# Kernel tuning notes

Hardware: AMD Instinct MI355X
Metric: run time of the kernel (lower is better)

The kernel has to match this reference:

```python
import jax, jax.numpy as jnp
import numpy as np

CAR_DIM = 8
ESC_MAX_AGENT = 32
HID = 256
ACTION_DIM = 30
NUM_STATES = 64
BATCH = 8192
ENC_OUT = 1 + CAR_DIM * ESC_MAX_AGENT          # 257
Q_IN = 1 + CAR_DIM + CAR_DIM * ESC_MAX_AGENT   # 265


def setup_inputs() -> dict:
    key = jax.random.key(0)
    ks = jax.random.split(key, 9)
    s = jax.random.normal(ks[0], (BATCH, CAR_DIM + NUM_STATES * CAR_DIM), dtype=jnp.float32)
    def lin(k, fan_in, fan_out):
        bound = 1.0 / np.sqrt(fan_in)
        kw, kb = jax.random.split(k)
        W = jax.random.uniform(kw, (fan_in, fan_out), jnp.float32, -bound, bound)
        b = jax.random.uniform(kb, (fan_out,), jnp.float32, -bound, bound)
        return W, b
    W1, b1 = lin(ks[1], CAR_DIM, HID)
    W2, b2 = lin(ks[2], HID, ENC_OUT)
    Qw1, Qb1 = lin(ks[3], Q_IN, HID)
    Qw2, Qb2 = lin(ks[4], HID, ACTION_DIM)
    return {"s": s, "W1": W1, "b1": b1, "W2": W2, "b2": b2,
            "Qw1": Qw1, "Qb1": Qb1, "Qw2": Qw2, "Qb2": Qb2}


def reference(s, W1, b1, W2, b2, Qw1, Qb1, Qw2, Qb2):
    B = s.shape[0]
    self_states = s[:, :CAR_DIM]                                   # [B, C]
    surr = s[:, CAR_DIM:].reshape(B, -1, CAR_DIM)                  # [B, N, C]
    # sentinel agents: any coordinate exactly == -1 is skipped
    valid = ~jnp.any(surr == -1.0, axis=-1)                        # [B, N] bool
    h = jax.nn.relu(jnp.einsum('bnc,ch->bnh', surr, W1) + b1)      # [B, N, HID]
    enc = jax.nn.relu(jnp.einsum('bnh,he->bne', h, W2) + b2)       # [B, N, ENC_OUT]
    sum_outputs = jnp.sum(enc * valid[:, :, None].astype(enc.dtype), axis=1)  # [B, ENC_OUT]
    x = jnp.concatenate([self_states, sum_outputs], axis=1)        # [B, Q_IN]
    q = jax.nn.relu(x @ Qw1 + Qb1) @ Qw2 + Qb2                     # [B, ACTION_DIM]
    return q
```

## Files before the change

kernel.cpp:

```cpp
#include <hip/hip_runtime.h>

#define CAR 8
#define SROW 520
#define HID 256
#define EOUT 257
#define XPAD 288
#define ADIM 30

typedef __attribute__((ext_vector_type(8))) short sh8;
typedef __attribute__((ext_vector_type(4))) float f32x4;

__device__ __forceinline__ short f2bf(float f) {
  unsigned u = __builtin_bit_cast(unsigned, f);
  u += 0x7fffu + ((u >> 16) & 1u);
  return (short)(u >> 16);
}
__device__ __forceinline__ unsigned f2bf2(float a, float b) {
  unsigned ua = __builtin_bit_cast(unsigned, a);
  ua += 0x7fffu + ((ua >> 16) & 1u);
  unsigned ub = __builtin_bit_cast(unsigned, b);
  ub += 0x7fffu + ((ub >> 16) & 1u);
  return __builtin_amdgcn_perm(ub, ua, 0x07060302);
}

__global__ void k_prep(const float* __restrict__ W1, const float* __restrict__ W2,
                       const float* __restrict__ Qw1, const float* __restrict__ Qw2,
                       short* __restrict__ w1f, short* __restrict__ w2f,
                       short* __restrict__ w3f, short* __restrict__ wq2f) {
  int idx = blockIdx.x * 256 + threadIdx.x;
  if (idx < 8192) {
    int mt = idx >> 9, r = idx & 511, lane = r >> 3, j = r & 7;
    int quad = lane >> 4, m = lane & 15;
    float v = (quad == 0) ? W1[j * HID + mt * 16 + m] : 0.0f;
    w1f[idx] = f2bf(v);
    return;
  }
  int i2 = idx - 8192;
  if (i2 < 69632) {
    int ks = i2 / 8704, r = i2 % 8704;
    int nt = r >> 9, r2 = r & 511, lane = r2 >> 3, j = r2 & 7;
    int quad = lane >> 4, m = lane & 15;
    int k = ks * 32 + quad * 8 + j, n = nt * 16 + m;
    float v = (n < EOUT) ? W2[k * EOUT + n] : 0.0f;
    w2f[i2] = f2bf(v);
    return;
  }
  int i3 = i2 - 69632;
  if (i3 < 73728) {
    int ks = i3 >> 13, r = i3 & 8191;
    int nt = r >> 9, r2 = r & 511, lane = r2 >> 3, j = r2 & 7;
    int quad = lane >> 4, m = lane & 15;
    int k = ks * 32 + quad * 8 + j, n = nt * 16 + m;
    float v = (k < 265) ? Qw1[k * HID + n] : 0.0f;
    w3f[i3] = f2bf(v);
    return;
  }
  int i4 = i3 - 73728;
  if (i4 < 8192) {
    int ks = i4 >> 10, r = i4 & 1023;
    int nt = r >> 9, r2 = r & 511, lane = r2 >> 3, j = r2 & 7;
    int quad = lane >> 4, m = lane & 15;
    int k = ks * 32 + quad * 8 + j, n = nt * 16 + m;
    float v = (n < ADIM) ? Qw2[k * ADIM + n] : 0.0f;
    wq2f[i4] = f2bf(v);
  }
}

__global__ __launch_bounds__(256, 2)
void k_enc(const float* __restrict__ s, const short* __restrict__ w1f,
           const float* __restrict__ b1, const short* __restrict__ w2f,
           const float* __restrict__ b2, float* __restrict__ so288) {
  __shared__ short hlds[16384];
  __shared__ float ninvp[4];

  const int b = blockIdx.x;
  const int tid = threadIdx.x;
  const int w = tid >> 6, lane = tid & 63;
  const int q = lane >> 4, m = lane & 15;
  const float* srow0 = s + (size_t)b * SROW + CAR;

  sh8 bs = {0, 0, 0, 0, 0, 0, 0, 0};
  bool inv = false;
  if (q == 0) {
    const float* sr = srow0 + (w * 16 + m) * CAR;
    float4 f0 = ((const float4*)sr)[0], f1 = ((const float4*)sr)[1];
    inv = (f0.x == -1.f) | (f0.y == -1.f) | (f0.z == -1.f) | (f0.w == -1.f) |
          (f1.x == -1.f) | (f1.y == -1.f) | (f1.z == -1.f) | (f1.w == -1.f);
    unsigned u0 = f2bf2(f0.x, f0.y), u1 = f2bf2(f0.z, f0.w);
    unsigned u2 = f2bf2(f1.x, f1.y), u3 = f2bf2(f1.z, f1.w);
    int4 t = {(int)u0, (int)u1, (int)u2, (int)u3};
    bs = __builtin_bit_cast(sh8, t);
  }
  const float vflag = inv ? 0.f : 1.f;
  const float vv = __shfl(vflag, m, 64);
  unsigned long long bal = __ballot(inv);
  if (lane == 0) ninvp[w] = (float)__popcll(bal);

#pragma unroll
  for (int mt = 0; mt < 16; ++mt) {
    sh8 af = *(const sh8*)(w1f + (mt * 64 + lane) * 8);
    f32x4 z = {0.f, 0.f, 0.f, 0.f};
    f32x4 c = __builtin_amdgcn_mfma_f32_16x16x32_bf16(af, bs, z, 0, 0, 0);
    const int hidb = mt * 16 + q * 4;
    float4 b1v = *(const float4*)(b1 + hidb);
    const int ks = hidb >> 5, qB = (hidb >> 3) & 3, js = hidb & 7;
    unsigned p0 = f2bf2(fmaxf(c[0] + b1v.x, 0.f) * vv, fmaxf(c[1] + b1v.y, 0.f) * vv);
    unsigned p1 = f2bf2(fmaxf(c[2] + b1v.z, 0.f) * vv, fmaxf(c[3] + b1v.w, 0.f) * vv);
    uint2 pk = {p0, p1};
    *(uint2*)(hlds + ((w * 8 + ks) * 64 + qB * 16 + m) * 8 + js) = pk;
  }
  __syncthreads();

  const int NT = (w == 0) ? 5 : 4;
  int tiles[5];
#pragma unroll
  for (int i = 0; i < 4; ++i) tiles[i] = 4 * w + i;
  tiles[4] = 16;

  f32x4 acc[4][5];
#pragma unroll
  for (int mt = 0; mt < 4; ++mt)
#pragma unroll
    for (int i = 0; i < 5; ++i) {
      f32x4 z = {0.f, 0.f, 0.f, 0.f};
      acc[mt][i] = z;
    }

#pragma unroll
  for (int ks = 0; ks < 8; ++ks) {
    sh8 A[4];
#pragma unroll
    for (int mt = 0; mt < 4; ++mt)
      A[mt] = *(const sh8*)(hlds + ((mt * 8 + ks) * 64 + lane) * 8);
    sh8 Bf[5];
#pragma unroll
    for (int i = 0; i < 5; ++i)
      if (i < NT)
        Bf[i] = *(const sh8*)(w2f + ((ks * 17 + tiles[i]) * 64 + lane) * 8);
#pragma unroll
    for (int i = 0; i < 5; ++i)
      if (i < NT)
#pragma unroll
        for (int mt = 0; mt < 4; ++mt)
          acc[mt][i] = __builtin_amdgcn_mfma_f32_16x16x32_bf16(A[mt], Bf[i], acc[mt][i], 0, 0, 0);
  }

  const float ninv = ninvp[0] + ninvp[1] + ninvp[2] + ninvp[3];
#pragma unroll
  for (int i = 0; i < 5; ++i)
    if (i < NT) {
      const int col = tiles[i] * 16 + m;
      const float b2c = (col < EOUT) ? b2[col] : 0.f;
      float ssum = 0.f;
#pragma unroll
      for (int mt = 0; mt < 4; ++mt)
#pragma unroll
        for (int r = 0; r < 4; ++r)
          ssum += fmaxf(acc[mt][i][r] + b2c, 0.f);
      ssum += __shfl_xor(ssum, 16, 64);
      ssum += __shfl_xor(ssum, 32, 64);
      ssum -= ninv * fmaxf(b2c, 0.f);
      if (q == 0)
        so288[(size_t)b * XPAD + CAR + col] = ssum;
    }
  if (w == 1 && lane < CAR)
    so288[(size_t)b * XPAD + lane] = s[(size_t)b * SROW + lane];
  if (w == 2 && lane < 8)
    so288[(size_t)b * XPAD + 280 + lane] = 0.f;
}

__global__ __launch_bounds__(64, 2)
void k_q(const float* __restrict__ so288, const short* __restrict__ w3f,
         const float* __restrict__ Qb1, const short* __restrict__ wq2f,
         const float* __restrict__ Qb2, float* __restrict__ out, int B) {
  __shared__ float H[16 * 260];
  const int lane = threadIdx.x;
  const int q = lane >> 4, m = lane & 15;
  const int b0 = blockIdx.x * 16;
  int row = b0 + m; if (row >= B) row = B - 1;
  const float* xr = so288 + (size_t)row * XPAD;

  f32x4 acc1[16];
#pragma unroll
  for (int nt = 0; nt < 16; ++nt) {
    f32x4 z = {0.f, 0.f, 0.f, 0.f};
    acc1[nt] = z;
  }

#pragma unroll
  for (int ks = 0; ks < 9; ++ks) {
    const float* xp = xr + ks * 32 + q * 8;
    float4 xa = ((const float4*)xp)[0], xb = ((const float4*)xp)[1];
    unsigned u0 = f2bf2(xa.x, xa.y), u1 = f2bf2(xa.z, xa.w);
    unsigned u2 = f2bf2(xb.x, xb.y), u3 = f2bf2(xb.z, xb.w);
    int4 t = {(int)u0, (int)u1, (int)u2, (int)u3};
    sh8 A = __builtin_bit_cast(sh8, t);
#pragma unroll
    for (int nt = 0; nt < 16; ++nt) {
      sh8 Bf = *(const sh8*)(w3f + ((ks * 16 + nt) * 64 + lane) * 8);
      acc1[nt] = __builtin_amdgcn_mfma_f32_16x16x32_bf16(A, Bf, acc1[nt], 0, 0, 0);
    }
  }
#pragma unroll
  for (int nt = 0; nt < 16; ++nt) {
    const float bq = Qb1[nt * 16 + m];
#pragma unroll
    for (int r = 0; r < 4; ++r)
      H[(q * 4 + r) * 260 + nt * 16 + m] = fmaxf(acc1[nt][r] + bq, 0.f);
  }
  __syncthreads();

  f32x4 acc2[2];
#pragma unroll
  for (int nt = 0; nt < 2; ++nt) {
    f32x4 z = {0.f, 0.f, 0.f, 0.f};
    acc2[nt] = z;
  }
#pragma unroll
  for (int ks = 0; ks < 8; ++ks) {
    const float* hp = H + m * 260 + ks * 32 + q * 8;
    float4 ha = ((const float4*)hp)[0], hb = ((const float4*)hp)[1];
    unsigned u0 = f2bf2(ha.x, ha.y), u1 = f2bf2(ha.z, ha.w);
    unsigned u2 = f2bf2(hb.x, hb.y), u3 = f2bf2(hb.z, hb.w);
    int4 t = {(int)u0, (int)u1, (int)u2, (int)u3};
    sh8 A2 = __builtin_bit_cast(sh8, t);
#pragma unroll
    for (int nt = 0; nt < 2; ++nt) {
      sh8 Bf = *(const sh8*)(wq2f + ((ks * 2 + nt) * 64 + lane) * 8);
      acc2[nt] = __builtin_amdgcn_mfma_f32_16x16x32_bf16(A2, Bf, acc2[nt], 0, 0, 0);
    }
  }
#pragma unroll
  for (int nt = 0; nt < 2; ++nt) {
    const int act = nt * 16 + m;
    if (act < ADIM) {
      const float bq = Qb2[act];
#pragma unroll
      for (int r = 0; r < 4; ++r) {
        const int br = b0 + q * 4 + r;
        if (br < B) out[(size_t)br * ADIM + act] = acc2[nt][r] + bq;
      }
    }
  }
}

extern "C" void kernel_launch(void* const* d_in, const int* in_sizes, int n_in,
                              void* d_out, int out_size, void* d_ws, size_t ws_size,
                              hipStream_t stream) {
  const float* s   = (const float*)d_in[0];
  const float* W1  = (const float*)d_in[1];
  const float* b1  = (const float*)d_in[2];
  const float* W2  = (const float*)d_in[3];
  const float* b2  = (const float*)d_in[4];
  const float* Qw1 = (const float*)d_in[5];
  const float* Qb1 = (const float*)d_in[6];
  const float* Qw2 = (const float*)d_in[7];
  const float* Qb2 = (const float*)d_in[8];
  float* out = (float*)d_out;
  const int B = in_sizes[0] / SROW;

  char* wsb = (char*)d_ws;
  float* so288 = (float*)wsb;
  size_t off = (size_t)B * XPAD * sizeof(float);
  short* w1f  = (short*)(wsb + off);            off += 8192 * 2;
  short* w2f  = (short*)(wsb + off);            off += 69632 * 2;
  short* w3f  = (short*)(wsb + off);            off += 73728 * 2;
  short* wq2f = (short*)(wsb + off);

  const int prep_elems = 8192 + 69632 + 73728 + 8192;
  k_prep<<<(prep_elems + 255) / 256, 256, 0, stream>>>(W1, W2, Qw1, Qw2,
                                                       w1f, w2f, w3f, wq2f);
  k_enc<<<B, 256, 0, stream>>>(s, w1f, b1, w2f, b2, so288);
  k_q<<<(B + 15) / 16, 64, 0, stream>>>(so288, w3f, Qb1, wq2f, Qb2, out, B);
}
```

Baseline: 178.4 us.

## Process two batch rows per encoder block and widen Q-head blocks to 32 rows

k_enc now handles two batch elements per block, so each W2 fragment it loads is reused across both elements' hidden tiles. W2 fragments are also prefetched one k-step ahead. k_q moves from 64-thread/16-row blocks to 256-thread/32-row blocks, with the bf16-converted input staged in LDS and the Qw1 column tiles split across waves. This is meant to cut redundant weight traffic and raise per-block MFMA work, at the cost of more registers (acc doubles to 40 f32x4), more LDS, and a padded fifth W2 tile on non-zero waves that now costs extra MFMAs. k_enc also assumes an even B, since odd B is not guarded.

```diff
diff --git a/kernel.cpp b/kernel.cpp
--- a/kernel.cpp
+++ b/kernel.cpp
@@ -70,176 +70,216 @@
 void k_enc(const float* __restrict__ s, const short* __restrict__ w1f,
            const float* __restrict__ b1, const short* __restrict__ w2f,
            const float* __restrict__ b2, float* __restrict__ so288) {
-  __shared__ short hlds[16384];
+  __shared__ __align__(16) short hlds[2][16384];
   __shared__ float ninvp[4];
 
-  const int b = blockIdx.x;
   const int tid = threadIdx.x;
   const int w = tid >> 6, lane = tid & 63;
   const int q = lane >> 4, m = lane & 15;
-  const float* srow0 = s + (size_t)b * SROW + CAR;
-
-  sh8 bs = {0, 0, 0, 0, 0, 0, 0, 0};
+  const int be = w >> 1, half = w & 1;
+  const size_t b0 = 2 * (size_t)blockIdx.x;
+  const int bg = (int)b0 + be;
+
+  const float* srow0 = s + (size_t)bg * SROW + CAR;
+  int4 pk = {0, 0, 0, 0};
   bool inv = false;
-  if (q == 0) {
-    const float* sr = srow0 + (w * 16 + m) * CAR;
+  if (lane < 32) {
+    const float* sr = srow0 + (half * 32 + lane) * CAR;
     float4 f0 = ((const float4*)sr)[0], f1 = ((const float4*)sr)[1];
     inv = (f0.x == -1.f) | (f0.y == -1.f) | (f0.z == -1.f) | (f0.w == -1.f) |
           (f1.x == -1.f) | (f1.y == -1.f) | (f1.z == -1.f) | (f1.w == -1.f);
-    unsigned u0 = f2bf2(f0.x, f0.y), u1 = f2bf2(f0.z, f0.w);
-    unsigned u2 = f2bf2(f1.x, f1.y), u3 = f2bf2(f1.z, f1.w);
-    int4 t = {(int)u0, (int)u1, (int)u2, (int)u3};
-    bs = __builtin_bit_cast(sh8, t);
+    pk.x = (int)f2bf2(f0.x, f0.y); pk.y = (int)f2bf2(f0.z, f0.w);
+    pk.z = (int)f2bf2(f1.x, f1.y); pk.w = (int)f2bf2(f1.z, f1.w);
   }
   const float vflag = inv ? 0.f : 1.f;
-  const float vv = __shfl(vflag, m, 64);
   unsigned long long bal = __ballot(inv);
   if (lane == 0) ninvp[w] = (float)__popcll(bal);
 
+  int4 p0, p1;
+  p0.x = __shfl(pk.x, m, 64);      p0.y = __shfl(pk.y, m, 64);
+  p0.z = __shfl(pk.z, m, 64);      p0.w = __shfl(pk.w, m, 64);
+  p1.x = __shfl(pk.x, 16 + m, 64); p1.y = __shfl(pk.y, 16 + m, 64);
+  p1.z = __shfl(pk.z, 16 + m, 64); p1.w = __shfl(pk.w, 16 + m, 64);
+  const float vv0 = __shfl(vflag, m, 64);
+  const float vv1 = __shfl(vflag, 16 + m, 64);
+  if (q != 0) { p0.x = p0.y = p0.z = p0.w = 0; p1.x = p1.y = p1.z = p1.w = 0; }
+  sh8 bs0 = __builtin_bit_cast(sh8, p0);
+  sh8 bs1 = __builtin_bit_cast(sh8, p1);
+
+  const int T0 = half * 2, T1 = half * 2 + 1;
 #pragma unroll
   for (int mt = 0; mt < 16; ++mt) {
     sh8 af = *(const sh8*)(w1f + (mt * 64 + lane) * 8);
     f32x4 z = {0.f, 0.f, 0.f, 0.f};
-    f32x4 c = __builtin_amdgcn_mfma_f32_16x16x32_bf16(af, bs, z, 0, 0, 0);
+    f32x4 c0 = __builtin_amdgcn_mfma_f32_16x16x32_bf16(af, bs0, z, 0, 0, 0);
+    f32x4 c1 = __builtin_amdgcn_mfma_f32_16x16x32_bf16(af, bs1, z, 0, 0, 0);
     const int hidb = mt * 16 + q * 4;
     float4 b1v = *(const float4*)(b1 + hidb);
     const int ks = hidb >> 5, qB = (hidb >> 3) & 3, js = hidb & 7;
-    unsigned p0 = f2bf2(fmaxf(c[0] + b1v.x, 0.f) * vv, fmaxf(c[1] + b1v.y, 0.f) * vv);
-    unsigned p1 = f2bf2(fmaxf(c[2] + b1v.z, 0.f) * vv, fmaxf(c[3] + b1v.w, 0.f) * vv);
-    uint2 pk = {p0, p1};
-    *(uint2*)(hlds + ((w * 8 + ks) * 64 + qB * 16 + m) * 8 + js) = pk;
+    uint2 k0, k1;
+    k0.x = f2bf2(fmaxf(c0[0] + b1v.x, 0.f) * vv0, fmaxf(c0[1] + b1v.y, 0.f) * vv0);
+    k0.y = f2bf2(fmaxf(c0[2] + b1v.z, 0.f) * vv0, fmaxf(c0[3] + b1v.w, 0.f) * vv0);
+    k1.x = f2bf2(fmaxf(c1[0] + b1v.x, 0.f) * vv1, fmaxf(c1[1] + b1v.y, 0.f) * vv1);
+    k1.y = f2bf2(fmaxf(c1[2] + b1v.z, 0.f) * vv1, fmaxf(c1[3] + b1v.w, 0.f) * vv1);
+    *(uint2*)(&hlds[be][((T0 * 8 + ks) * 64 + qB * 16 + m) * 8 + js]) = k0;
+    *(uint2*)(&hlds[be][((T1 * 8 + ks) * 64 + qB * 16 + m) * 8 + js]) = k1;
   }
   __syncthreads();
 
-  const int NT = (w == 0) ? 5 : 4;
   int tiles[5];
 #pragma unroll
   for (int i = 0; i < 4; ++i) tiles[i] = 4 * w + i;
-  tiles[4] = 16;
-
-  f32x4 acc[4][5];
+  tiles[4] = (w == 0) ? 16 : 4 * w;
+
+  f32x4 acc[4][5][2];
 #pragma unroll
   for (int mt = 0; mt < 4; ++mt)
 #pragma unroll
-    for (int i = 0; i < 5; ++i) {
-      f32x4 z = {0.f, 0.f, 0.f, 0.f};
-      acc[mt][i] = z;
-    }
+    for (int i = 0; i < 5; ++i)
+#pragma unroll
+      for (int e = 0; e < 2; ++e) {
+        f32x4 z = {0.f, 0.f, 0.f, 0.f};
+        acc[mt][i][e] = z;
+      }
+
+  sh8 Bf[5];
+#pragma unroll
+  for (int i = 0; i < 5; ++i)
+    Bf[i] = *(const sh8*)(w2f + ((0 * 17 + tiles[i]) * 64 + lane) * 8);
 
 #pragma unroll
   for (int ks = 0; ks < 8; ++ks) {
-    sh8 A[4];
-#pragma unroll
-    for (int mt = 0; mt < 4; ++mt)
-      A[mt] = *(const sh8*)(hlds + ((mt * 8 + ks) * 64 + lane) * 8);
-    sh8 Bf[5];
-#pragma unroll
-    for (int i = 0; i < 5; ++i)
-      if (i < NT)
-        Bf[i] = *(const sh8*)(w2f + ((ks * 17 + tiles[i]) * 64 + lane) * 8);
-#pragma unroll
-    for (int i = 0; i < 5; ++i)
-      if (i < NT)
+    sh8 Bn[5];
+    if (ks < 7) {
+#pragma unroll
+      for (int i = 0; i < 5; ++i)
+        Bn[i] = *(const sh8*)(w2f + (((ks + 1) * 17 + tiles[i]) * 64 + lane) * 8);
+    }
+#pragma unroll
+    for (int e = 0; e < 2; ++e) {
+      sh8 A[4];
+#pragma unroll
+      for (int mt = 0; mt < 4; ++mt)
+        A[mt] = *(const sh8*)(&hlds[e][((mt * 8 + ks) * 64 + lane) * 8]);
+#pragma unroll
+      for (int i = 0; i < 5; ++i)
 #pragma unroll
         for (int mt = 0; mt < 4; ++mt)
-          acc[mt][i] = __builtin_amdgcn_mfma_f32_16x16x32_bf16(A[mt], Bf[i], acc[mt][i], 0, 0, 0);
-  }
-
-  const float ninv = ninvp[0] + ninvp[1] + ninvp[2] + ninvp[3];
-#pragma unroll
-  for (int i = 0; i < 5; ++i)
-    if (i < NT) {
-      const int col = tiles[i] * 16 + m;
-      const float b2c = (col < EOUT) ? b2[col] : 0.f;
+          acc[mt][i][e] = __builtin_amdgcn_mfma_f32_16x16x32_bf16(A[mt], Bf[i], acc[mt][i][e], 0, 0, 0);
+    }
+    if (ks < 7) {
+#pragma unroll
+      for (int i = 0; i < 5; ++i) Bf[i] = Bn[i];
+    }
+  }
+
+  const float ninv[2] = {ninvp[0] + ninvp[1], ninvp[2] + ninvp[3]};
+#pragma unroll
+  for (int i = 0; i < 5; ++i) {
+    if (i == 4 && w != 0) continue;
+    const int col = tiles[i] * 16 + m;
+    const float b2c = (col < EOUT) ? b2[col] : 0.f;
+    const float rb2 = fmaxf(b2c, 0.f);
+#pragma unroll
+    for (int e = 0; e < 2; ++e) {
       float ssum = 0.f;
 #pragma unroll
       for (int mt = 0; mt < 4; ++mt)
 #pragma unroll
         for (int r = 0; r < 4; ++r)
-          ssum += fmaxf(acc[mt][i][r] + b2c, 0.f);
+          ssum += fmaxf(acc[mt][i][e][r] + b2c, 0.f);
       ssum += __shfl_xor(ssum, 16, 64);
       ssum += __shfl_xor(ssum, 32, 64);
-      ssum -= ninv * fmaxf(b2c, 0.f);
+      ssum -= ninv[e] * rb2;
       if (q == 0)
-        so288[(size_t)b * XPAD + CAR + col] = ssum;
-    }
-  if (w == 1 && lane < CAR)
-    so288[(size_t)b * XPAD + lane] = s[(size_t)b * SROW + lane];
-  if (w == 2 && lane < 8)
-    so288[(size_t)b * XPAD + 280 + lane] = 0.f;
-}
-
-__global__ __launch_bounds__(64, 2)
+        so288[(b0 + e) * XPAD + CAR + col] = ssum;
+    }
+  }
+  if (w == 1 || w == 2) {
+    const size_t rr = b0 + (w - 1);
+    if (lane < CAR)       so288[rr * XPAD + lane] = s[rr * SROW + lane];
+    else if (lane < 16)   so288[rr * XPAD + 280 + (lane - 8)] = 0.f;
+  }
+}
+
+__global__ __launch_bounds__(256, 2)
 void k_q(const float* __restrict__ so288, const short* __restrict__ w3f,
          const float* __restrict__ Qb1, const short* __restrict__ wq2f,
          const float* __restrict__ Qb2, float* __restrict__ out, int B) {
-  __shared__ float H[16 * 260];
-  const int lane = threadIdx.x;
+  __shared__ __align__(16) short xf[2 * 9 * 64 * 8];
+  __shared__ __align__(16) float H[32 * 260];
+  const int tid = threadIdx.x;
+  const int w = tid >> 6, lane = tid & 63;
   const int q = lane >> 4, m = lane & 15;
-  const int b0 = blockIdx.x * 16;
-  int row = b0 + m; if (row >= B) row = B - 1;
-  const float* xr = so288 + (size_t)row * XPAD;
-
-  f32x4 acc1[16];
-#pragma unroll
-  for (int nt = 0; nt < 16; ++nt) {
-    f32x4 z = {0.f, 0.f, 0.f, 0.f};
-    acc1[nt] = z;
-  }
-
+  const int b0 = blockIdx.x * 32;
+
+#pragma unroll
+  for (int it = 0; it < 5; ++it) {
+    int sidx = tid + it * 256;
+    if (sidx < 1152) {
+      int mt = sidx / 576, rem = sidx % 576;
+      int ks = rem >> 6, l = rem & 63;
+      int lq = l >> 4, lm = l & 15;
+      int row = b0 + mt * 16 + lm; if (row >= B) row = B - 1;
+      const float* xp = so288 + (size_t)row * XPAD + ks * 32 + lq * 8;
+      float4 xa = ((const float4*)xp)[0], xb = ((const float4*)xp)[1];
+      int4 t = {(int)f2bf2(xa.x, xa.y), (int)f2bf2(xa.z, xa.w),
+                (int)f2bf2(xb.x, xb.y), (int)f2bf2(xb.z, xb.w)};
+      *(int4*)(xf + sidx * 8) = t;
+    }
+  }
+  __syncthreads();
+
+  f32x4 acc1[2][4];
+#pragma unroll
+  for (int mt = 0; mt < 2; ++mt)
+#pragma unroll
+    for (int i = 0; i < 4; ++i) {
+      f32x4 z = {0.f, 0.f, 0.f, 0.f};
+      acc1[mt][i] = z;
+    }
 #pragma unroll
   for (int ks = 0; ks < 9; ++ks) {
-    const float* xp = xr + ks * 32 + q * 8;
-    float4 xa = ((const float4*)xp)[0], xb = ((const float4*)xp)[1];
-    unsigned u0 = f2bf2(xa.x, xa.y), u1 = f2bf2(xa.z, xa.w);
-    unsigned u2 = f2bf2(xb.x, xb.y), u3 = f2bf2(xb.z, xb.w);
-    int4 t = {(int)u0, (int)u1, (int)u2, (int)u3};
-    sh8 A = __builtin_bit_cast(sh8, t);
-#pragma unroll
-    for (int nt = 0; nt < 16; ++nt) {
-      sh8 Bf = *(const sh8*)(w3f + ((ks * 16 + nt) * 64 + lane) * 8);
-      acc1[nt] = __builtin_amdgcn_mfma_f32_16x16x32_bf16(A, Bf, acc1[nt], 0, 0, 0);
-    }
-  }
-#pragma unroll
-  for (int nt = 0; nt < 16; ++nt) {
-    const float bq = Qb1[nt * 16 + m];
-#pragma unroll
-    for (int r = 0; r < 4; ++r)
-      H[(q * 4 + r) * 260 + nt * 16 + m] = fmaxf(acc1[nt][r] + bq, 0.f);
+    sh8 A0 = *(const sh8*)(xf + ((0 * 9 + ks) * 64 + lane) * 8);
+    sh8 A1 = *(const sh8*)(xf + ((1 * 9 + ks) * 64 + lane) * 8);
+#pragma unroll
+    for (int i = 0; i < 4; ++i) {
+      sh8 Bf = *(const sh8*)(w3f + ((ks * 16 + 4 * w + i) * 64 + lane) * 8);
+      acc1[0][i] = __builtin_amdgcn_mfma_f32_16x16x32_bf16(A0, Bf, acc1[0][i], 0, 0, 0);
+      acc1[1][i] = __builtin_amdgcn_mfma_f32_16x16x32_bf16(A1, Bf, acc1[1][i], 0, 0, 0);
+    }
+  }
+#pragma unroll
+  for (int i = 0; i < 4; ++i) {
+    const int hcol = (4 * w + i) * 16 + m;
+    const float bq = Qb1[hcol];
+#pragma unroll
+    for (int mt = 0; mt < 2; ++mt)
+#pragma unroll
+      for (int r = 0; r < 4; ++r)
+        H[(mt * 16 + q * 4 + r) * 260 + hcol] = fmaxf(acc1[mt][i][r] + bq, 0.f);
   }
   __syncthreads();
 
-  f32x4 acc2[2];
-#pragma unroll
-  for (int nt = 0; nt < 2; ++nt) {
-    f32x4 z = {0.f, 0.f, 0.f, 0.f};
-    acc2[nt] = z;
-  }
+  const int mt2 = w >> 1, nt2 = w & 1;
+  f32x4 acc2 = {0.f, 0.f, 0.f, 0.f};
 #pragma unroll
   for (int ks = 0; ks < 8; ++ks) {
-    const float* hp = H + m * 260 + ks * 32 + q * 8;
+    const float* hp = H + (mt2 * 16 + m) * 260 + ks * 32 + q * 8;
     float4 ha = ((const float4*)hp)[0], hb = ((const float4*)hp)[1];
-    unsigned u0 = f2bf2(ha.x, ha.y), u1 = f2bf2(ha.z, ha.w);
-    unsigned u2 = f2bf2(hb.x, hb.y), u3 = f2bf2(hb.z, hb.w);
-    int4 t = {(int)u0, (int)u1, (int)u2, (int)u3};
+    int4 t = {(int)f2bf2(ha.x, ha.y), (int)f2bf2(ha.z, ha.w),
+              (int)f2bf2(hb.x, hb.y), (int)f2bf2(hb.z, hb.w)};
     sh8 A2 = __builtin_bit_cast(sh8, t);
-#pragma unroll
-    for (int nt = 0; nt < 2; ++nt) {
-      sh8 Bf = *(const sh8*)(wq2f + ((ks * 2 + nt) * 64 + lane) * 8);
-      acc2[nt] = __builtin_amdgcn_mfma_f32_16x16x32_bf16(A2, Bf, acc2[nt], 0, 0, 0);
-    }
-  }
-#pragma unroll
-  for (int nt = 0; nt < 2; ++nt) {
-    const int act = nt * 16 + m;
-    if (act < ADIM) {
-      const float bq = Qb2[act];
-#pragma unroll
-      for (int r = 0; r < 4; ++r) {
-        const int br = b0 + q * 4 + r;
-        if (br < B) out[(size_t)br * ADIM + act] = acc2[nt][r] + bq;
-      }
+    sh8 Bf = *(const sh8*)(wq2f + ((ks * 2 + nt2) * 64 + lane) * 8);
+    acc2 = __builtin_amdgcn_mfma_f32_16x16x32_bf16(A2, Bf, acc2, 0, 0, 0);
+  }
+  const int act = nt2 * 16 + m;
+  if (act < ADIM) {
+    const float bq = Qb2[act];
+#pragma unroll
+    for (int r = 0; r < 4; ++r) {
+      const int row = b0 + mt2 * 16 + q * 4 + r;
+      if (row < B) out[(size_t)row * ADIM + act] = acc2[r] + bq;
     }
   }
 }
@@ -270,6 +310,6 @@
   const int prep_elems = 8192 + 69632 + 73728 + 8192;
   k_prep<<<(prep_elems + 255) / 256, 256, 0, stream>>>(W1, W2, Qw1, Qw2,
                                                        w1f, w2f, w3f, wq2f);
-  k_enc<<<B, 256, 0, stream>>>(s, w1f, b1, w2f, b2, so288);
-  k_q<<<(B + 15) / 16, 64, 0, stream>>>(so288, w3f, Qb1, wq2f, Qb2, out, B);
-}
+  k_enc<<<(B + 1) / 2, 256, 0, stream>>>(s, w1f, b1, w2f, b2, so288);
+  k_q<<<(B + 31) / 32, 256, 0, stream>>>(so288, w3f, Qb1, wq2f, Qb2, out, B);
+}
```

After: 168.7 us. 1.06x faster.
